# Optimization experiments

Hardware: AMD Instinct MI355X
Metric: run time of the kernel (lower is better)

Reference implementation:

```python
import jax, jax.numpy as jnp
import numpy as np

IN_DIM = 100000   # entity vocab
H_DIM = 128       # h_dim == dist_dim (forced in __init__)
K = 16            # num_neighbor
BOUNDARIES = jnp.array([1.0, 2.0, 4.0, 8.0, 16.0, 32.0, 64.0, 128.0], dtype=jnp.float32)
N_BUCKETS = BOUNDARIES.shape[0] + 1


def setup_inputs() -> dict:
    key = jax.random.key(0)
    ks = jax.random.split(key, 8)
    N = 100000
    node_ids = jax.random.randint(ks[0], (N,), 0, IN_DIM)
    nbr_idx = jax.random.randint(ks[1], (N, K), 0, N)
    nbr_dist = jax.random.uniform(ks[2], (N, K), dtype=jnp.float32) * 200.0
    scale = 1.0 / np.sqrt(H_DIM)
    embed_table = jax.random.normal(ks[3], (IN_DIM, H_DIM), dtype=jnp.float32) * scale
    dist_table = jax.random.normal(ks[4], (N_BUCKETS, H_DIM), dtype=jnp.float32) * scale
    W_self = jax.random.normal(ks[5], (H_DIM, H_DIM), dtype=jnp.float32) * scale
    W_nbr = jax.random.normal(ks[6], (H_DIM, H_DIM), dtype=jnp.float32) * scale
    b = jnp.zeros((H_DIM,), dtype=jnp.float32)
    return {
        "node_ids": node_ids, "nbr_idx": nbr_idx, "nbr_dist": nbr_dist,
        "embed_table": embed_table, "dist_table": dist_table,
        "W_self": W_self, "W_nbr": W_nbr, "b": b,
    }


def reference(node_ids, nbr_idx, nbr_dist, embed_table, dist_table, W_self, W_nbr, b):
    # h = self.embedding(h.squeeze())
    h = embed_table[node_ids]                       # [N, D] gather
    # DistRelConv: gather sampled neighbor features
    neigh = h[nbr_idx]                              # [N, K, D] gather
    # bucketize edge distances against boundaries -> distance-bucket embedding
    bucket = jnp.searchsorted(BOUNDARIES, nbr_dist) # [N, K] int
    msg = neigh + dist_table[bucket]                # [N, K, D]
    agg = jnp.mean(msg, axis=1)                     # [N, D]
    # merge='sum': self transform + neighbor transform, relu activation
    out = jax.nn.relu(h @ W_self + agg @ W_nbr + b) # [N, D]
    return out
```

## Files before the change

### kernel.cpp

```cpp
#include <hip/hip_runtime.h>
#include <stdint.h>

#define KNBR 16
#define STAGE_D 6

typedef float f32x4 __attribute__((ext_vector_type(4)));
typedef float f32x2 __attribute__((ext_vector_type(2)));
typedef __bf16 bf16x8 __attribute__((ext_vector_type(8)));

union ABFrag { uint4 u; bf16x8 v; };

__device__ __forceinline__ uint32_t bf16_rne(float x) {
    uint32_t u = __float_as_uint(x);
    return (u + 0x7fffu + ((u >> 16) & 1u)) >> 16;
}

__device__ __forceinline__ uint32_t bucket_of(float d) {
    uint32_t u = __float_as_uint(d);
    int e = (int)((u >> 23) & 0xff) - 127;
    int b = e + ((u & 0x7fffffu) != 0 ? 1 : 0);
    return (uint32_t)min(max(b, 0), 8);
}

#define GLD(gsrc, ldst)                                                          \
    __builtin_amdgcn_global_load_lds(                                            \
        (const __attribute__((address_space(1))) void*)(gsrc),                   \
        (__attribute__((address_space(3))) void*)(ldst), 4, 0, 0)

__global__ void k_prep(const float* __restrict__ src, uint32_t* __restrict__ ebf,
                       uint32_t* __restrict__ e8, int n_dwords,
                       const float* __restrict__ Ws, const float* __restrict__ Wn,
                       uint16_t* __restrict__ Bp) {
    if (blockIdx.x < 2048) {
        int i = blockIdx.x * blockDim.x + threadIdx.x;
        int stride = 2048 * blockDim.x;
        for (; i < n_dwords; i += stride) {
            float4 v = ((const float4*)src)[i];
            ebf[2 * i]     = bf16_rne(v.x) | (bf16_rne(v.y) << 16);
            ebf[2 * i + 1] = bf16_rne(v.z) | (bf16_rne(v.w) << 16);
            uint32_t p = 0;
            p = __builtin_amdgcn_cvt_pk_fp8_f32(v.x, v.y, p, false);
            p = __builtin_amdgcn_cvt_pk_fp8_f32(v.z, v.w, p, true);
            e8[i] = p;
        }
    } else {
        int o = (blockIdx.x - 2048) * blockDim.x + threadIdx.x;
        if (o >= 8 * 8 * 64 * 8) return;
        int i = o & 7, lane = (o >> 3) & 63, nt = (o >> 9) & 7, ks = o >> 12;
        int r = ks * 32 + (lane >> 4) * 8 + i;
        int c = nt * 16 + (lane & 15);
        float v = (r < 128) ? Ws[r * 128 + c] : Wn[(r - 128) * 128 + c];
        Bp[o] = (uint16_t)bf16_rne(v);
    }
}

__global__ __launch_bounds__(256, 2) void k_fused(
    const int* __restrict__ node_ids, const int* __restrict__ nbr_idx,
    const float* __restrict__ nbr_dist,
    const uint32_t* __restrict__ emb_bf, const uint16_t* __restrict__ emb8,
    const float* __restrict__ dist_table, const float* __restrict__ bias,
    const uint32_t* __restrict__ Bp, float* __restrict__ out, int ntiles)
{
    __shared__ uint32_t As[4 * 16 * 128];
    __shared__ uint32_t Ss[4 * STAGE_D * 512];

    const int lane = threadIdx.x & 63;
    const int w = threadIdx.x >> 6;
    const int l_hi = lane >> 4;
    const int l_lo = lane & 15;
    uint32_t* Aw = As + w * 2048;
    uint32_t* Sw = Ss + w * (STAGE_D * 512);
    float* Fw = (float*)Aw;

    const int tile = blockIdx.x * 4 + w;
    if (tile >= ntiles) return;

    float2 dreg[9];
    #pragma unroll
    for (int b = 0; b < 9; ++b)
        dreg[b] = *(const float2*)(dist_table + b * 128 + 2 * lane);
    float breg[8];
    #pragma unroll
    for (int nt = 0; nt < 8; ++nt) breg[nt] = bias[nt * 16 + l_lo];

    int4 nb = *(const int4*)(nbr_idx + (size_t)tile * 256 + lane * 4);
    float4 dd = *(const float4*)(nbr_dist + (size_t)tile * 256 + lane * 4);
    uint32_t ea[4];
    ea[0] = ((uint32_t)node_ids[nb.x] & 0xFFFFFFu) | (bucket_of(dd.x) << 24);
    ea[1] = ((uint32_t)node_ids[nb.y] & 0xFFFFFFu) | (bucket_of(dd.y) << 24);
    ea[2] = ((uint32_t)node_ids[nb.z] & 0xFFFFFFu) | (bucket_of(dd.z) << 24);
    ea[3] = ((uint32_t)node_ids[nb.w] & 0xFFFFFFu) | (bucket_of(dd.w) << 24);
    uint32_t selfv = (uint32_t)node_ids[(size_t)tile * 16 + (lane & 15)];

#define ISSUE(J) do {                                                                     \
        const int sw_ = ((J) & 7) << 2;                                                   \
        const uint32_t sid_ = (uint32_t)__builtin_amdgcn_readlane((int)selfv, (J));       \
        GLD(emb_bf + (size_t)sid_ * 64 + (lane ^ sw_), Aw + (J) * 128);                   \
        uint32_t* sb_ = Sw + ((J) % STAGE_D) * 512;                                       \
        _Pragma("unroll")                                                                 \
        for (int m = 0; m < 8; ++m) {                                                     \
            const int L_ = 4 * (J) + (m >> 1);                                            \
            const uint32_t s0_ = (uint32_t)__builtin_amdgcn_readlane((int)ea[(2*m) & 3], L_) & 0xFFFFFFu;   \
            const uint32_t s1_ = (uint32_t)__builtin_amdgcn_readlane((int)ea[(2*m+1) & 3], L_) & 0xFFFFFFu; \
            const uint32_t sel_ = (lane < 32) ? s0_ : s1_;                                \
            GLD((const uint8_t*)emb8 + (size_t)sel_ * 128 + (lane & 31) * 4, sb_ + m * 64); \
        }                                                                                 \
    } while (0)

#define CONSUME(J, VM) do {                                                               \
        asm volatile("s_waitcnt vmcnt(" #VM ")" ::: "memory");                            \
        const uint16_t* st_ = (const uint16_t*)(Sw + ((J) % STAGE_D) * 512);              \
        float ax = 0.f, ay = 0.f;                                                         \
        uint64_t c_ = 0;                                                                  \
        _Pragma("unroll")                                                                 \
        for (int k = 0; k < KNBR; ++k) {                                                  \
            const uint32_t ew_ = (uint32_t)__builtin_amdgcn_readlane((int)ea[k & 3], 4 * (J) + (k >> 2)); \
            c_ += 1ull << (5 * (ew_ >> 24));                                              \
            const uint32_t pv_ = (uint32_t)st_[k * 64 + lane];                            \
            f32x2 d_ = __builtin_amdgcn_cvt_pk_f32_fp8(pv_, false);                       \
            ax += d_.x; ay += d_.y;                                                       \
        }                                                                                 \
        _Pragma("unroll")                                                                 \
        for (int b = 0; b < 9; ++b) {                                                     \
            const float fb_ = (float)(uint32_t)((c_ >> (5 * b)) & 31u);                   \
            ax += fb_ * dreg[b].x; ay += fb_ * dreg[b].y;                                 \
        }                                                                                 \
        ax *= 0.0625f; ay *= 0.0625f;                                                     \
        const int sw_ = ((J) & 7) << 2;                                                   \
        Aw[(J) * 128 + (64 + (lane ^ sw_))] = bf16_rne(ax) | (bf16_rne(ay) << 16);        \
        __builtin_amdgcn_sched_barrier(0);                                                \
    } while (0)

    ISSUE(0); ISSUE(1); ISSUE(2); ISSUE(3); ISSUE(4); ISSUE(5);
    CONSUME(0, 45);  ISSUE(6);
    CONSUME(1, 45);  ISSUE(7);
    CONSUME(2, 45);  ISSUE(8);
    CONSUME(3, 45);  ISSUE(9);
    CONSUME(4, 45);  ISSUE(10);
    CONSUME(5, 45);  ISSUE(11);
    CONSUME(6, 45);  ISSUE(12);
    CONSUME(7, 45);  ISSUE(13);
    CONSUME(8, 45);  ISSUE(14);
    CONSUME(9, 45);  ISSUE(15);
    CONSUME(10, 45);
    CONSUME(11, 36);
    CONSUME(12, 27);
    CONSUME(13, 18);
    CONSUME(14, 9);
    CONSUME(15, 0);
#undef ISSUE
#undef CONSUME

    asm volatile("s_waitcnt vmcnt(0) lgkmcnt(0)" ::: "memory");
    __builtin_amdgcn_sched_barrier(0);

    f32x4 acc[8];
    #pragma unroll
    for (int t = 0; t < 8; ++t) acc[t] = (f32x4){0.f, 0.f, 0.f, 0.f};
    #pragma unroll
    for (int ks = 0; ks < 8; ++ks) {
        ABFrag a;
        a.u = *(const uint4*)(Aw + l_lo * 128 + ((ks * 16 + l_hi * 4) ^ ((l_lo & 7) << 2)));
        #pragma unroll
        for (int nt = 0; nt < 8; ++nt) {
            ABFrag b;
            b.u = ((const uint4*)Bp)[(ks * 8 + nt) * 64 + lane];
            acc[nt] = __builtin_amdgcn_mfma_f32_16x16x32_bf16(a.v, b.v, acc[nt], 0, 0, 0);
        }
    }

    #pragma unroll
    for (int nt = 0; nt < 8; ++nt) {
        const int col = nt * 16 + l_lo;
        #pragma unroll
        for (int r = 0; r < 4; ++r) {
            const int row = l_hi * 4 + r;
            float v = acc[nt][r] + breg[nt];
            Fw[row * 128 + (col ^ ((row & 7) << 2))] = v > 0.f ? v : 0.f;
        }
    }
    float* dst = out + (size_t)tile * 2048;
    #pragma unroll
    for (int it = 0; it < 8; ++it) {
        const int f = it * 256 + lane * 4;
        const int r = f >> 7, c = f & 127;
        float4 v = *(const float4*)(Fw + r * 128 + (c ^ ((r & 7) << 2)));
        *(float4*)(dst + f) = v;
    }
}

__global__ void k_naive(const int* __restrict__ node_ids, const int* __restrict__ nbr_idx,
                        const float* __restrict__ nbr_dist, const float* __restrict__ emb,
                        const float* __restrict__ dt, const float* __restrict__ Ws,
                        const float* __restrict__ Wn, const float* __restrict__ bias,
                        float* __restrict__ out, int base) {
    __shared__ float h[128], ag[128];
    const int nd = base + blockIdx.x;
    const int t = threadIdx.x;
    const int nid = node_ids[nd];
    float hv = emb[(size_t)nid * 128 + t];
    float a = 0.f;
    for (int k = 0; k < KNBR; ++k) {
        int sn = node_ids[nbr_idx[(size_t)nd * KNBR + k]];
        int bkt = (int)bucket_of(nbr_dist[(size_t)nd * KNBR + k]);
        a += emb[(size_t)sn * 128 + t] + dt[bkt * 128 + t];
    }
    h[t] = hv; ag[t] = a * 0.0625f;
    __syncthreads();
    float s = bias[t];
    for (int d = 0; d < 128; ++d) s += h[d] * Ws[d * 128 + t] + ag[d] * Wn[d * 128 + t];
    out[(size_t)nd * 128 + t] = s > 0.f ? s : 0.f;
}

extern "C" void kernel_launch(void* const* d_in, const int* in_sizes, int n_in,
                              void* d_out, int out_size, void* d_ws, size_t ws_size,
                              hipStream_t stream) {
    const int* node_ids   = (const int*)d_in[0];
    const int* nbr_idx    = (const int*)d_in[1];
    const float* nbr_dist = (const float*)d_in[2];
    const float* emb      = (const float*)d_in[3];
    const float* dist_tab = (const float*)d_in[4];
    const float* Ws       = (const float*)d_in[5];
    const float* Wn       = (const float*)d_in[6];
    const float* bias     = (const float*)d_in[7];
    float* out = (float*)d_out;
    const int n = in_sizes[0];
    const int in_dim = in_sizes[3] / 128;

    const size_t offEbf = 65536;
    const size_t offE8  = offEbf + (size_t)in_dim * 256;
    const size_t needT  = offE8 + (size_t)in_dim * 128;

    if (ws_size < needT) {
        if (n > 0)
            k_naive<<<n, 128, 0, stream>>>(node_ids, nbr_idx, nbr_dist, emb, dist_tab, Ws, Wn, bias, out, 0);
        return;
    }
    uint16_t* Bp   = (uint16_t*)d_ws;
    uint32_t* ebf  = (uint32_t*)((char*)d_ws + offEbf);
    uint32_t* e8   = (uint32_t*)((char*)d_ws + offE8);

    k_prep<<<2176, 256, 0, stream>>>(emb, ebf, e8, in_dim * 32, Ws, Wn, Bp);

    const int ntiles = n >> 4;
    const int rem = n & 15;

    if (ntiles > 0) {
        const int nblocks = (ntiles + 3) >> 2;
        k_fused<<<nblocks, 256, 0, stream>>>(node_ids, nbr_idx, nbr_dist, ebf, (const uint16_t*)e8,
                                             dist_tab, bias, (const uint32_t*)Bp, out, ntiles);
    }
    if (rem > 0)
        k_naive<<<rem, 128, 0, stream>>>(node_ids, nbr_idx, nbr_dist, emb, dist_tab, Ws, Wn, bias, out, ntiles << 4);
}
```

Baseline: 94.02 us.

## Halve rows per wave and shrink LDS staging to raise occupancy

Each wave now processes 8 nodes instead of 16, and the per-wave LDS footprint is cut by sharing one buffer for the A tile and a 3-deep neighbor staging ring. Launch bounds rise to 4 blocks per CU. The goal is more resident waves to hide the latency of the random embedding gathers. In exchange, half of each 16-row MFMA tile is wasted on rows that are discarded, weight-fragment loads per node double, and each wave has a shallower prefetch pipeline.

```diff
diff --git a/kernel.cpp b/kernel.cpp
--- a/kernel.cpp
+++ b/kernel.cpp
@@ -2,7 +2,6 @@
 #include <stdint.h>
 
 #define KNBR 16
-#define STAGE_D 6
 
 typedef float f32x4 __attribute__((ext_vector_type(4)));
 typedef float f32x2 __attribute__((ext_vector_type(2)));
@@ -54,26 +53,25 @@
     }
 }
 
-__global__ __launch_bounds__(256, 2) void k_fused(
+__global__ __launch_bounds__(256, 4) void k_fused(
     const int* __restrict__ node_ids, const int* __restrict__ nbr_idx,
     const float* __restrict__ nbr_dist,
     const uint32_t* __restrict__ emb_bf, const uint16_t* __restrict__ emb8,
     const float* __restrict__ dist_table, const float* __restrict__ bias,
-    const uint32_t* __restrict__ Bp, float* __restrict__ out, int ntiles)
+    const uint32_t* __restrict__ Bp, float* __restrict__ out, int nht)
 {
-    __shared__ uint32_t As[4 * 16 * 128];
-    __shared__ uint32_t Ss[4 * STAGE_D * 512];
+    __shared__ uint32_t L[4 * 2560];
 
     const int lane = threadIdx.x & 63;
     const int w = threadIdx.x >> 6;
     const int l_hi = lane >> 4;
     const int l_lo = lane & 15;
-    uint32_t* Aw = As + w * 2048;
-    uint32_t* Sw = Ss + w * (STAGE_D * 512);
+    uint32_t* Aw = L + w * 2560;
+    uint32_t* Sw = Aw + 1024;
     float* Fw = (float*)Aw;
 
-    const int tile = blockIdx.x * 4 + w;
-    if (tile >= ntiles) return;
+    const int ht = blockIdx.x * 4 + w;
+    if (ht >= nht) return;
 
     float2 dreg[9];
     #pragma unroll
@@ -83,25 +81,24 @@
     #pragma unroll
     for (int nt = 0; nt < 8; ++nt) breg[nt] = bias[nt * 16 + l_lo];
 
-    int4 nb = *(const int4*)(nbr_idx + (size_t)tile * 256 + lane * 4);
-    float4 dd = *(const float4*)(nbr_dist + (size_t)tile * 256 + lane * 4);
-    uint32_t ea[4];
+    int2 nb = *(const int2*)(nbr_idx + (size_t)ht * 128 + lane * 2);
+    float2 dd = *(const float2*)(nbr_dist + (size_t)ht * 128 + lane * 2);
+    uint32_t ea[2];
     ea[0] = ((uint32_t)node_ids[nb.x] & 0xFFFFFFu) | (bucket_of(dd.x) << 24);
     ea[1] = ((uint32_t)node_ids[nb.y] & 0xFFFFFFu) | (bucket_of(dd.y) << 24);
-    ea[2] = ((uint32_t)node_ids[nb.z] & 0xFFFFFFu) | (bucket_of(dd.z) << 24);
-    ea[3] = ((uint32_t)node_ids[nb.w] & 0xFFFFFFu) | (bucket_of(dd.w) << 24);
-    uint32_t selfv = (uint32_t)node_ids[(size_t)tile * 16 + (lane & 15)];
+    uint32_t selfv = (uint32_t)node_ids[(size_t)ht * 8 + (lane & 7)];
+
 
 #define ISSUE(J) do {                                                                     \
         const int sw_ = ((J) & 7) << 2;                                                   \
         const uint32_t sid_ = (uint32_t)__builtin_amdgcn_readlane((int)selfv, (J));       \
         GLD(emb_bf + (size_t)sid_ * 64 + (lane ^ sw_), Aw + (J) * 128);                   \
-        uint32_t* sb_ = Sw + ((J) % STAGE_D) * 512;                                       \
+        uint32_t* sb_ = Sw + ((J) % 3) * 512;                                             \
         _Pragma("unroll")                                                                 \
         for (int m = 0; m < 8; ++m) {                                                     \
-            const int L_ = 4 * (J) + (m >> 1);                                            \
-            const uint32_t s0_ = (uint32_t)__builtin_amdgcn_readlane((int)ea[(2*m) & 3], L_) & 0xFFFFFFu;   \
-            const uint32_t s1_ = (uint32_t)__builtin_amdgcn_readlane((int)ea[(2*m+1) & 3], L_) & 0xFFFFFFu; \
+            const int L_ = 8 * (J) + m;                                                   \
+            const uint32_t s0_ = (uint32_t)__builtin_amdgcn_readlane((int)ea[0], L_) & 0xFFFFFFu; \
+            const uint32_t s1_ = (uint32_t)__builtin_amdgcn_readlane((int)ea[1], L_) & 0xFFFFFFu; \
             const uint32_t sel_ = (lane < 32) ? s0_ : s1_;                                \
             GLD((const uint8_t*)emb8 + (size_t)sel_ * 128 + (lane & 31) * 4, sb_ + m * 64); \
         }                                                                                 \
@@ -109,12 +106,12 @@
 
 #define CONSUME(J, VM) do {                                                               \
         asm volatile("s_waitcnt vmcnt(" #VM ")" ::: "memory");                            \
-        const uint16_t* st_ = (const uint16_t*)(Sw + ((J) % STAGE_D) * 512);              \
+        const uint16_t* st_ = (const uint16_t*)(Sw + ((J) % 3) * 512);                    \
         float ax = 0.f, ay = 0.f;                                                         \
         uint64_t c_ = 0;                                                                  \
         _Pragma("unroll")                                                                 \
         for (int k = 0; k < KNBR; ++k) {                                                  \
-            const uint32_t ew_ = (uint32_t)__builtin_amdgcn_readlane((int)ea[k & 3], 4 * (J) + (k >> 2)); \
+            const uint32_t ew_ = (uint32_t)__builtin_amdgcn_readlane((int)ea[k & 1], 8 * (J) + (k >> 1)); \
             c_ += 1ull << (5 * (ew_ >> 24));                                              \
             const uint32_t pv_ = (uint32_t)st_[k * 64 + lane];                            \
             f32x2 d_ = __builtin_amdgcn_cvt_pk_f32_fp8(pv_, false);                       \
@@ -131,23 +128,15 @@
         __builtin_amdgcn_sched_barrier(0);                                                \
     } while (0)
 
-    ISSUE(0); ISSUE(1); ISSUE(2); ISSUE(3); ISSUE(4); ISSUE(5);
-    CONSUME(0, 45);  ISSUE(6);
-    CONSUME(1, 45);  ISSUE(7);
-    CONSUME(2, 45);  ISSUE(8);
-    CONSUME(3, 45);  ISSUE(9);
-    CONSUME(4, 45);  ISSUE(10);
-    CONSUME(5, 45);  ISSUE(11);
-    CONSUME(6, 45);  ISSUE(12);
-    CONSUME(7, 45);  ISSUE(13);
-    CONSUME(8, 45);  ISSUE(14);
-    CONSUME(9, 45);  ISSUE(15);
-    CONSUME(10, 45);
-    CONSUME(11, 36);
-    CONSUME(12, 27);
-    CONSUME(13, 18);
-    CONSUME(14, 9);
-    CONSUME(15, 0);
+    ISSUE(0); ISSUE(1); ISSUE(2);
+    CONSUME(0, 18);  ISSUE(3);
+    CONSUME(1, 18);  ISSUE(4);
+    CONSUME(2, 18);  ISSUE(5);
+    CONSUME(3, 18);  ISSUE(6);
+    CONSUME(4, 18);  ISSUE(7);
+    CONSUME(5, 18);
+    CONSUME(6, 9);
+    CONSUME(7, 0);
 #undef ISSUE
 #undef CONSUME
 
@@ -175,13 +164,15 @@
         #pragma unroll
         for (int r = 0; r < 4; ++r) {
             const int row = l_hi * 4 + r;
-            float v = acc[nt][r] + breg[nt];
-            Fw[row * 128 + (col ^ ((row & 7) << 2))] = v > 0.f ? v : 0.f;
+            if (row < 8) {
+                float v = acc[nt][r] + breg[nt];
+                Fw[row * 128 + (col ^ ((row & 7) << 2))] = v > 0.f ? v : 0.f;
+            }
         }
     }
-    float* dst = out + (size_t)tile * 2048;
-    #pragma unroll
-    for (int it = 0; it < 8; ++it) {
+    float* dst = out + (size_t)ht * 1024;
+    #pragma unroll
+    for (int it = 0; it < 4; ++it) {
         const int f = it * 256 + lane * 4;
         const int r = f >> 7, c = f & 127;
         float4 v = *(const float4*)(Fw + r * 128 + (c ^ ((r & 7) << 2)));
@@ -242,14 +233,14 @@
 
     k_prep<<<2176, 256, 0, stream>>>(emb, ebf, e8, in_dim * 32, Ws, Wn, Bp);
 
-    const int ntiles = n >> 4;
-    const int rem = n & 15;
-
-    if (ntiles > 0) {
-        const int nblocks = (ntiles + 3) >> 2;
+    const int nht = n >> 3;
+    const int rem = n & 7;
+
+    if (nht > 0) {
+        const int nblocks = (nht + 3) >> 2;
         k_fused<<<nblocks, 256, 0, stream>>>(node_ids, nbr_idx, nbr_dist, ebf, (const uint16_t*)e8,
-                                             dist_tab, bias, (const uint32_t*)Bp, out, ntiles);
+                                             dist_tab, bias, (const uint32_t*)Bp, out, nht);
     }
     if (rem > 0)
-        k_naive<<<rem, 128, 0, stream>>>(node_ids, nbr_idx, nbr_dist, emb, dist_tab, Ws, Wn, bias, out, ntiles << 4);
-}
+        k_naive<<<rem, 128, 0, stream>>>(node_ids, nbr_idx, nbr_dist, emb, dist_tab, Ws, Wn, bias, out, nht << 3);
+}
```

New measurement: 82.86 us. -11.9%, faster.
